# Optimization experiments

Measured on AMD Instinct MI355X. Metric: run time of the kernel, lower is better.

## Reference

```python
import jax, jax.numpy as jnp
import numpy as np

D_MODEL = 1024
N_HEAD = 16
DK = D_MODEL // N_HEAD


def setup_inputs() -> dict:
    key = jax.random.key(0)
    ks = jax.random.split(key, 9)
    s = 1.0 / np.sqrt(D_MODEL)
    x = jax.random.normal(ks[0], (2, 2048, D_MODEL), dtype=jnp.float32)
    def lin(kw, kb):
        W = jax.random.uniform(kw, (D_MODEL, D_MODEL), minval=-s, maxval=s, dtype=jnp.float32)
        b = jax.random.uniform(kb, (D_MODEL,), minval=-s, maxval=s, dtype=jnp.float32)
        return W, b
    Wq, bq = lin(ks[1], ks[2])
    Wk, bk = lin(ks[3], ks[4])
    Wv, bv = lin(ks[5], ks[6])
    Wo, bo = lin(ks[7], ks[8])
    return {"x": x, "Wq": Wq, "bq": bq, "Wk": Wk, "bk": bk,
            "Wv": Wv, "bv": bv, "Wo": Wo, "bo": bo}


def reference(x, Wq, bq, Wk, bk, Wv, bv, Wo, bo):
    B, T, _ = x.shape
    # nn.Linear: x @ W.T + b; reshape to (B, H, T, dk)
    def proj(W, b):
        y = x @ W.T + b
        return y.reshape(B, T, N_HEAD, DK).transpose(0, 2, 1, 3)
    Q = proj(Wq, bq)
    K = proj(Wk, bk)
    V = proj(Wv, bv)
    scores = jnp.einsum('bhqd,bhkd->bhqk', Q, K) / jnp.sqrt(jnp.float32(DK))
    attn = jax.nn.softmax(scores, axis=-1)
    out = jnp.einsum('bhqk,bhkd->bhqd', attn, V)
    out = out.transpose(0, 2, 1, 3).reshape(B, T, D_MODEL)
    return out @ Wo.T + bo
```

## Files before the change

kernel.cpp:

```cpp
#include <hip/hip_runtime.h>
#include <hip/hip_bf16.h>
#include <cstdint>

typedef unsigned short u16;
typedef __attribute__((ext_vector_type(8))) __bf16 bf16x8;
typedef __attribute__((ext_vector_type(8))) short s16x8;
typedef __attribute__((ext_vector_type(4))) short s16x4;
typedef __attribute__((ext_vector_type(4))) float f32x4;
typedef __attribute__((ext_vector_type(4))) unsigned u32x4;

#define T_SEQ 2048
#define D_MODEL 1024
#define MROWS 4096
#define QSCALE (0.125f * 1.44269504088896f)

__device__ __forceinline__ u16 f2bf(float f) {
  unsigned u = __builtin_bit_cast(unsigned, f);
  u += 0x7fffu + ((u >> 16) & 1u);
  return (u16)(u >> 16);
}

__device__ __forceinline__ unsigned cvt_pk_bf16(float lo, float hi) {
  unsigned r;
  asm("v_cvt_pk_bf16_f32 %0, %1, %2" : "=v"(r) : "v"(lo), "v"(hi));
  return r;
}

__device__ __forceinline__ void plswap(unsigned& a, unsigned& b) {
  asm("v_permlane32_swap_b32 %0, %1" : "+v"(a), "+v"(b));
  asm("v_permlane16_swap_b32 %0, %1" : "+v"(a), "+v"(b));
}

__device__ __forceinline__ void gld_lds16(const void* g, void* l) {
  __builtin_amdgcn_global_load_lds(
      (__attribute__((address_space(1))) void*)(uintptr_t)(g),
      (__attribute__((address_space(3))) void*)(uintptr_t)(l), 16, 0, 0);
}

__device__ __forceinline__ f32x4 mfma16(s16x8 a, s16x8 b, f32x4 c) {
  return __builtin_amdgcn_mfma_f32_16x16x32_bf16(
      __builtin_bit_cast(bf16x8, a), __builtin_bit_cast(bf16x8, b), c, 0, 0, 0);
}

__global__ __launch_bounds__(256) void cvt5(
    const float* __restrict__ x,
    const float* __restrict__ w0, const float* __restrict__ w1,
    const float* __restrict__ w2, const float* __restrict__ w3,
    u16* __restrict__ dx, u16* __restrict__ dw0, u16* __restrict__ dw1,
    u16* __restrict__ dw2, u16* __restrict__ dw3) {
  const int NX = (MROWS * D_MODEL) / 4;
  const int NW = (D_MODEL * D_MODEL) / 4;
  int i = blockIdx.x * 256 + threadIdx.x;
  const float* s;
  u16* d;
  int off;
  if (i < NX) {
    s = x; d = dx; off = i;
  } else {
    int j = i - NX;
    int r = j >> 18;
    off = j & (NW - 1);
    if (r == 0) { s = w0; d = dw0; }
    else if (r == 1) { s = w1; d = dw1; }
    else if (r == 2) { s = w2; d = dw2; }
    else { s = w3; d = dw3; }
  }
  float4 v = ((const float4*)s)[off];
  uint2 o;
  o.x = cvt_pk_bf16(v.x, v.y);
  o.y = cvt_pk_bf16(v.z, v.w);
  ((uint2*)d)[off] = o;
}

__global__ __launch_bounds__(512, 2) void gemm_qkv(const u16* __restrict__ A,
    const u16* __restrict__ Wf,
    const float* __restrict__ bq, const float* __restrict__ bk, const float* __restrict__ bv,
    u16* __restrict__ Qo, u16* __restrict__ Ko, u16* __restrict__ Vo) {
  __shared__ char smem[131072];

  const int t = threadIdx.x;
  const int lane = t & 63;
  const int lq = lane & 15, g = lane >> 4;
  const int w = t >> 6;
  const int wm = w >> 2, wn = w & 3;

  const int f = blockIdx.x;
  const int xcd = f & 7, i = f >> 3;
  const int by = (xcd & 3) * 4 + (i & 3);
  const int bx = (xcd >> 2) * 6 + (i >> 2);
  const int bm2 = by * 256, bn2 = bx * 256;

  auto stage = [&](int dst, int mat, int kh, int kt2) {
    const u16* gbase = mat ? Wf : A;
    const int gr0 = mat ? bn2 : bm2;
    char* lbase = smem + (((dst << 1) + mat) * 2 + kh) * 16384;
#pragma unroll
    for (int s = 0; s < 2; ++s) {
      const int idx = s * 512 + t;
      const int row = idx >> 2, c16 = idx & 3;
      const int gcol = kt2 * 64 + kh * 32 + 8 * (c16 ^ ((row >> 1) & 3));
      gld_lds16(gbase + (size_t)(gr0 + row) * D_MODEL + gcol, lbase + idx * 16);
    }
  };

  f32x4 acc[8][4] = {};
  const int swz4 = ((lq >> 1) & 3) << 4;
  const int aoff0 = (wm * 128 + lq) * 64 + ((g * 16) ^ swz4);
  const int boff0 = (wn * 64 + lq) * 64 + ((g * 16) ^ swz4);

  s16x8 bfr[4];
  auto loadB = [&](const char* cb) {
#pragma unroll
    for (int fc = 0; fc < 4; ++fc)
      bfr[fc] = *(const s16x8*)(cb + boff0 + fc * 1024);
  };
  auto quad = [&](const char* ca, int fr0) {
    s16x8 a[4];
#pragma unroll
    for (int ii = 0; ii < 4; ++ii)
      a[ii] = *(const s16x8*)(ca + aoff0 + (fr0 + ii) * 1024);
    __builtin_amdgcn_s_setprio(1);
#pragma unroll
    for (int ii = 0; ii < 4; ++ii)
#pragma unroll
      for (int fc = 0; fc < 4; ++fc)
        acc[fr0 + ii][fc] = mfma16(a[ii], bfr[fc], acc[fr0 + ii][fc]);
    __builtin_amdgcn_s_setprio(0);
  };

  stage(0, 0, 0, 0);
  stage(0, 1, 0, 0);
  stage(0, 0, 1, 0);
  stage(0, 1, 1, 0);

  const int NT = D_MODEL / 64;
#pragma unroll 1
  for (int kt = 0; kt < NT; ++kt) {
    const int d = kt & 1;
    const char* A0 = smem + (((d << 1) + 0) * 2 + 0) * 16384;
    const char* A1 = smem + (((d << 1) + 0) * 2 + 1) * 16384;
    const char* B0 = smem + (((d << 1) + 1) * 2 + 0) * 16384;
    const char* B1 = smem + (((d << 1) + 1) * 2 + 1) * 16384;
    const bool more = kt + 1 < NT;

    asm volatile("s_waitcnt vmcnt(4)" ::: "memory");
    __builtin_amdgcn_s_barrier();
    if (more) stage(d ^ 1, 0, 0, kt + 1);
    loadB(B0);
    quad(A0, 0);
    if (more) stage(d ^ 1, 1, 0, kt + 1);
    quad(A0, 4);

    if (more) asm volatile("s_waitcnt vmcnt(4)" ::: "memory");
    else      asm volatile("s_waitcnt vmcnt(0)" ::: "memory");
    __builtin_amdgcn_s_barrier();
    if (more) stage(d ^ 1, 0, 1, kt + 1);
    loadB(B1);
    quad(A1, 0);
    if (more) stage(d ^ 1, 1, 1, kt + 1);
    quad(A1, 4);
  }

  const int z = bn2 >> 10;
  const float* bias = z == 0 ? bq : (z == 1 ? bk : bv);
  u16* out = z == 0 ? Qo : (z == 1 ? Ko : Vo);
  const float scale = z == 0 ? QSCALE : 1.0f;
  const int bnl = bn2 & 1023;
#pragma unroll
  for (int fc = 0; fc < 4; ++fc) {
    const int col = bnl + wn * 64 + fc * 16 + lq;
    const float bvv = bias[col];
#pragma unroll
    for (int fr = 0; fr < 8; ++fr) {
      const int row0 = bm2 + wm * 128 + fr * 16 + g * 4;
#pragma unroll
      for (int r = 0; r < 4; ++r)
        out[(size_t)(row0 + r) * D_MODEL + col] = f2bf((acc[fr][fc][r] + bvv) * scale);
    }
  }
}

template <int BN, class Epi>
__device__ __forceinline__ void gemm_pipe(const u16* __restrict__ A,
    const u16* __restrict__ Bw, const int K, const int bm, const int bn, Epi epi) {
  constexpr int NJ = BN / 32;
  constexpr int VM = 2 + BN / 64;
  constexpr int AB = 8192;
  __shared__ char lds[3][AB + BN * 64];
  const int t = threadIdx.x;
  const int lane = t & 63;
  const int lq = lane & 15, g = lane >> 4;
  const int w = t >> 6;
  const int wr = w >> 1, wc = w & 1;

  f32x4 acc[4][NJ] = {};
  const int NT = K >> 5;

  auto stage = [&](int buf, int kt) {
    const int k0 = kt << 5;
#pragma unroll
    for (int s = 0; s < 2; ++s) {
      const int idx = s * 256 + t;
      const int kk = idx >> 7, mm = idx & 127;
      gld_lds16(A + (size_t)(bm + mm) * K + (k0 + kk * 8), &lds[buf][(idx & ~63) * 16]);
    }
#pragma unroll
    for (int s = 0; s < BN / 64; ++s) {
      const int idx = s * 256 + t;
      const int kk = idx / BN, nn = idx % BN;
      gld_lds16(Bw + (size_t)(bn + nn) * K + (k0 + kk * 8), &lds[buf][AB + (idx & ~63) * 16]);
    }
  };

  auto compute = [&](int buf) {
    const char* la = &lds[buf][0];
    const char* lb = &lds[buf][AB];
    s16x8 af[4], bfr[NJ];
#pragma unroll
    for (int i = 0; i < 4; ++i)
      af[i] = *(const s16x8*)(la + g * 2048 + (wr * 64 + i * 16 + lq) * 16);
#pragma unroll
    for (int j = 0; j < NJ; ++j)
      bfr[j] = *(const s16x8*)(lb + g * (BN * 16) + (wc * (BN / 2) + j * 16 + lq) * 16);
    __builtin_amdgcn_s_setprio(1);
#pragma unroll
    for (int i = 0; i < 4; ++i)
#pragma unroll
      for (int j = 0; j < NJ; ++j)
        acc[i][j] = mfma16(af[i], bfr[j], acc[i][j]);
    __builtin_amdgcn_s_setprio(0);
  };

  auto vmwait = [&]() {
    if constexpr (VM == 4) asm volatile("s_waitcnt vmcnt(4)" ::: "memory");
    else asm volatile("s_waitcnt vmcnt(3)" ::: "memory");
  };

  stage(0, 0);
  stage(1, 1);
  int b0 = 0, b1 = 1, b2 = 2;
#pragma unroll 1
  for (int kt = 0; kt < NT - 2; ++kt) {
    vmwait();
    __builtin_amdgcn_s_barrier();
    stage(b2, kt + 2);
    compute(b0);
    const int tmp = b0; b0 = b1; b1 = b2; b2 = tmp;
  }
  vmwait();
  __builtin_amdgcn_s_barrier();
  compute(b0);
  asm volatile("s_waitcnt vmcnt(0)" ::: "memory");
  __builtin_amdgcn_s_barrier();
  compute(b1);

  epi(acc, lq, g, wr, wc);
}

__global__ __launch_bounds__(256) void gemm_out(const u16* __restrict__ A,
    const u16* __restrict__ W, const float* __restrict__ bias, float* __restrict__ C) {
  const int f = blockIdx.x;
  const int xcd = f & 7, i = f >> 3;
  const int by = xcd * 4 + (i & 3);
  const int bx = i >> 2;
  const int bm = by * 128, bn = bx * 64;

  gemm_pipe<64>(A, W, D_MODEL, bm, bn,
      [&](f32x4 (&acc)[4][2], int lq, int g, int wr, int wc) {
#pragma unroll
        for (int j = 0; j < 2; ++j) {
          const int col = bn + wc * 32 + j * 16 + lq;
          const float bvv = bias[col];
#pragma unroll
          for (int i2 = 0; i2 < 4; ++i2) {
            const int row0 = bm + wr * 64 + i2 * 16 + g * 4;
#pragma unroll
            for (int r = 0; r < 4; ++r)
              C[(size_t)(row0 + r) * D_MODEL + col] = acc[i2][j][r] + bvv;
          }
        }
      });
}

__global__ __launch_bounds__(512, 4) void attn_kernel(const u16* __restrict__ Qw,
    const u16* __restrict__ Kw, const u16* __restrict__ Vw, u16* __restrict__ AO) {
  __shared__ char smem[34816];
  char* Ks = smem;
  char* Vs = smem + 16384;

  const int t = threadIdx.x;
  const int w = t >> 6, lane = t & 63;
  const int lq = lane & 15, g = lane >> 4;
  const int qh = w >> 1, kh = w & 1;

  const int flat = blockIdx.y * 16 + blockIdx.x;
  const int xcd = flat & 7, idx = flat >> 3;
  const int bh = xcd * 4 + (idx & 3);
  const int qt = idx >> 2;
  const int b = bh >> 4, h = bh & 15;
  const size_t headoff = (size_t)b * T_SEQ * D_MODEL + h * 64;
  const int swz = (lq & 7) << 4;

  s16x8 qf[2][2];
#pragma unroll
  for (int qb = 0; qb < 2; ++qb) {
    const u16* qptr = Qw + headoff + (size_t)(qt * 128 + qh * 32 + qb * 16 + lq) * D_MODEL;
#pragma unroll
    for (int hb = 0; hb < 2; ++hb)
      qf[qb][hb] = *(const s16x8*)(qptr + hb * 32 + g * 8);
  }

  const int kkey = t >> 3, kslot = t & 7;
  auto stageK = [&](int buf, int kt) {
    const int d0 = 8 * (kslot ^ (kkey & 7));
    gld_lds16(Kw + headoff + (size_t)(kt * 64 + kkey) * D_MODEL + d0,
              Ks + buf * 8192 + (t & ~63) * 16);
  };

  const int kp = t & 31, dg = t >> 5;
  auto loadV = [&](int kt, s16x4& va, s16x4& vb2) {
    const u16* gv = Vw + headoff + (size_t)(kt * 64 + 2 * kp) * D_MODEL + 4 * dg;
    va = *(const s16x4*)gv;
    vb2 = *(const s16x4*)(gv + D_MODEL);
  };
  auto writeV = [&](int buf, s16x4 va, s16x4 vb2) {
    char* vbase = Vs + buf * 8192;
#pragma unroll
    for (int j = 0; j < 4; ++j) {
      const int d = 4 * dg + j;
      const unsigned u = (unsigned)(u16)va[j] | ((unsigned)(u16)vb2[j] << 16);
      *(unsigned*)(vbase + d * 128 + ((4 * kp) ^ ((d & 7) << 4))) = u;
    }
  };

  f32x4 o[4][2] = {};
  f32x4 lsum[2] = {};

  s16x4 va, vb2;
  stageK(0, 0);
  loadV(0, va, vb2);

  int cur = 0;
#pragma unroll 1
  for (int kt = 0; kt < T_SEQ / 64; ++kt) {
    asm volatile("s_waitcnt vmcnt(0)" ::: "memory");
    writeV(cur, va, vb2);
    __syncthreads();
    const bool more = kt + 1 < T_SEQ / 64;
    if (more) { stageK(cur ^ 1, kt + 1); loadV(kt + 1, va, vb2); }

    const char* kb_ = Ks + cur * 8192 + kh * 4096;
    f32x4 s[2][2] = {};
    __builtin_amdgcn_s_setprio(1);
#pragma unroll
    for (int kb = 0; kb < 2; ++kb)
#pragma unroll
      for (int hb = 0; hb < 2; ++hb) {
        const s16x8 kf = *(const s16x8*)(kb_ + (16 * kb + lq) * 128 + ((64 * hb + 16 * g) ^ swz));
#pragma unroll
        for (int qb = 0; qb < 2; ++qb)
          s[kb][qb] = mfma16(kf, qf[qb][hb], s[kb][qb]);
      }
    __builtin_amdgcn_s_setprio(0);

#pragma unroll
    for (int kb = 0; kb < 2; ++kb)
#pragma unroll
      for (int qb = 0; qb < 2; ++qb) {
#pragma unroll
        for (int r = 0; r < 4; ++r) s[kb][qb][r] = __builtin_amdgcn_exp2f(s[kb][qb][r]);
        lsum[qb] += s[kb][qb];
      }

    s16x8 pb[2];
#pragma unroll
    for (int qb = 0; qb < 2; ++qb) {
      unsigned a0 = cvt_pk_bf16(s[0][qb][0], s[0][qb][1]);
      unsigned a1 = cvt_pk_bf16(s[0][qb][2], s[0][qb][3]);
      unsigned b0 = cvt_pk_bf16(s[1][qb][0], s[1][qb][1]);
      unsigned b1 = cvt_pk_bf16(s[1][qb][2], s[1][qb][3]);
      plswap(a0, b0);
      plswap(a1, b1);
      u32x4 pk = {a0, a1, b0, b1};
      pb[qb] = __builtin_bit_cast(s16x8, pk);
    }

    const char* vb_ = Vs + cur * 8192;
    __builtin_amdgcn_s_setprio(1);
#pragma unroll
    for (int f = 0; f < 4; ++f) {
      const s16x8 av = *(const s16x8*)(vb_ + (16 * f + lq) * 128 + ((64 * kh + 16 * g) ^ swz));
#pragma unroll
      for (int qb = 0; qb < 2; ++qb)
        o[f][qb] = mfma16(av, pb[qb], o[f][qb]);
    }
    __builtin_amdgcn_s_setprio(0);
    cur ^= 1;
  }

  float rsq[2];
#pragma unroll
  for (int qb = 0; qb < 2; ++qb) {
    float r_ = lsum[qb][0] + lsum[qb][1] + lsum[qb][2] + lsum[qb][3];
    r_ += __shfl_xor(r_, 16);
    r_ += __shfl_xor(r_, 32);
    rsq[qb] = r_;
  }

  __syncthreads();
  char* obuf = smem;
  float* rbuf = (float*)(smem + 32768);
  if (kh == 1) {
#pragma unroll
    for (int f = 0; f < 4; ++f)
#pragma unroll
      for (int qb = 0; qb < 2; ++qb)
        *(f32x4*)(obuf + qh * 8192 + lane * 128 + (((f * 2 + qb) * 16) ^ ((lane & 7) << 4))) =
            o[f][qb];
    rbuf[qh * 128 + lane * 2 + 0] = rsq[0];
    rbuf[qh * 128 + lane * 2 + 1] = rsq[1];
  }
  __syncthreads();
  if (kh == 0) {
#pragma unroll
    for (int f = 0; f < 4; ++f)
#pragma unroll
      for (int qb = 0; qb < 2; ++qb)
        o[f][qb] += *(const f32x4*)(obuf + qh * 8192 + lane * 128 +
                                    (((f * 2 + qb) * 16) ^ ((lane & 7) << 4)));
    const float inv0 = 1.0f / (rsq[0] + rbuf[qh * 128 + lane * 2 + 0]);
    const float inv1 = 1.0f / (rsq[1] + rbuf[qh * 128 + lane * 2 + 1]);
#pragma unroll
    for (int qb = 0; qb < 2; ++qb) {
      const float inv = qb ? inv1 : inv0;
      u16* orow = AO + headoff + (size_t)(qt * 128 + qh * 32 + qb * 16 + lq) * D_MODEL;
#pragma unroll
      for (int f = 0; f < 4; ++f) {
        uint2 ov;
        ov.x = cvt_pk_bf16(o[f][qb][0] * inv, o[f][qb][1] * inv);
        ov.y = cvt_pk_bf16(o[f][qb][2] * inv, o[f][qb][3] * inv);
        *(uint2*)(orow + 16 * f + 4 * g) = ov;
      }
    }
  }
}

extern "C" void kernel_launch(void* const* d_in, const int* in_sizes, int n_in,
                              void* d_out, int out_size, void* d_ws, size_t ws_size,
                              hipStream_t stream) {
  const float* x  = (const float*)d_in[0];
  const float* Wq = (const float*)d_in[1];
  const float* bq = (const float*)d_in[2];
  const float* Wk = (const float*)d_in[3];
  const float* bk = (const float*)d_in[4];
  const float* Wv = (const float*)d_in[5];
  const float* bv = (const float*)d_in[6];
  const float* Wo = (const float*)d_in[7];
  const float* bo = (const float*)d_in[8];

  char* ws = (char*)d_ws;
  const size_t MB = 1u << 20;
  u16* x_bf  = (u16*)(ws + 0 * MB);
  u16* AO    = x_bf;
  u16* Wq_bf = (u16*)(ws + 8 * MB);
  u16* Wk_bf = (u16*)(ws + 10 * MB);
  u16* Wv_bf = (u16*)(ws + 12 * MB);
  u16* Wo_bf = (u16*)(ws + 14 * MB);
  u16* Qs  = (u16*)(ws + 16 * MB);
  u16* Ksb = (u16*)(ws + 24 * MB);
  u16* Vsb = (u16*)(ws + 32 * MB);

  const int NCVT = (MROWS * D_MODEL + 4 * D_MODEL * D_MODEL) / 4;
  cvt5<<<NCVT / 256, 256, 0, stream>>>(x, Wq, Wk, Wv, Wo,
                                       x_bf, Wq_bf, Wk_bf, Wv_bf, Wo_bf);

  gemm_qkv<<<192, 512, 0, stream>>>(x_bf, Wq_bf, bq, bk, bv, Qs, Ksb, Vsb);
  attn_kernel<<<dim3(16, 32), 512, 0, stream>>>(Qs, Ksb, Vsb, AO);
  gemm_out<<<512, 256, 0, stream>>>(AO, Wo_bf, bo, (float*)d_out);
}
```

Baseline: 117.7 us.

## Restructure QKV GEMM into triple-buffered 32-wide K pipeline with less LDS

Replaces the double-buffered 64-wide K-tile loop in the QKV projection GEMM with a three-stage ring of 32-wide K tiles, cutting shared memory from 128KB to 96KB. Each iteration loads A and B fragments, issues prefetch of the tile two steps ahead, and splits the MFMA work into two halves separated by barriers. The aim is deeper prefetch and lower LDS use. In exchange it adds more barriers per unit of K work and relies on the vmcnt accounting being right.

```diff
diff --git a/kernel.cpp b/kernel.cpp
--- a/kernel.cpp
+++ b/kernel.cpp
@@ -76,7 +76,7 @@
     const u16* __restrict__ Wf,
     const float* __restrict__ bq, const float* __restrict__ bk, const float* __restrict__ bv,
     u16* __restrict__ Qo, u16* __restrict__ Ko, u16* __restrict__ Vo) {
-  __shared__ char smem[131072];
+  __shared__ char smem[98304];
 
   const int t = threadIdx.x;
   const int lane = t & 63;
@@ -90,15 +90,15 @@
   const int bx = (xcd >> 2) * 6 + (i >> 2);
   const int bm2 = by * 256, bn2 = bx * 256;
 
-  auto stage = [&](int dst, int mat, int kh, int kt2) {
+  auto stage = [&](int b, int mat, int kt) {
     const u16* gbase = mat ? Wf : A;
     const int gr0 = mat ? bn2 : bm2;
-    char* lbase = smem + (((dst << 1) + mat) * 2 + kh) * 16384;
+    char* lbase = smem + b * 32768 + mat * 16384;
 #pragma unroll
     for (int s = 0; s < 2; ++s) {
       const int idx = s * 512 + t;
       const int row = idx >> 2, c16 = idx & 3;
-      const int gcol = kt2 * 64 + kh * 32 + 8 * (c16 ^ ((row >> 1) & 3));
+      const int gcol = kt * 32 + 8 * (c16 ^ ((row >> 1) & 3));
       gld_lds16(gbase + (size_t)(gr0 + row) * D_MODEL + gcol, lbase + idx * 16);
     }
   };
@@ -108,57 +108,49 @@
   const int aoff0 = (wm * 128 + lq) * 64 + ((g * 16) ^ swz4);
   const int boff0 = (wn * 64 + lq) * 64 + ((g * 16) ^ swz4);
 
-  s16x8 bfr[4];
-  auto loadB = [&](const char* cb) {
-#pragma unroll
-    for (int fc = 0; fc < 4; ++fc)
-      bfr[fc] = *(const s16x8*)(cb + boff0 + fc * 1024);
-  };
-  auto quad = [&](const char* ca, int fr0) {
-    s16x8 a[4];
-#pragma unroll
-    for (int ii = 0; ii < 4; ++ii)
-      a[ii] = *(const s16x8*)(ca + aoff0 + (fr0 + ii) * 1024);
-    __builtin_amdgcn_s_setprio(1);
-#pragma unroll
-    for (int ii = 0; ii < 4; ++ii)
-#pragma unroll
-      for (int fc = 0; fc < 4; ++fc)
-        acc[fr0 + ii][fc] = mfma16(a[ii], bfr[fc], acc[fr0 + ii][fc]);
-    __builtin_amdgcn_s_setprio(0);
-  };
-
-  stage(0, 0, 0, 0);
-  stage(0, 1, 0, 0);
-  stage(0, 0, 1, 0);
-  stage(0, 1, 1, 0);
-
-  const int NT = D_MODEL / 64;
+  stage(0, 0, 0); stage(0, 1, 0);
+  stage(1, 0, 1); stage(1, 1, 1);
+  asm volatile("s_waitcnt vmcnt(4)" ::: "memory");
+  __builtin_amdgcn_s_barrier();
+
+  const int NT = 32;
 #pragma unroll 1
   for (int kt = 0; kt < NT; ++kt) {
-    const int d = kt & 1;
-    const char* A0 = smem + (((d << 1) + 0) * 2 + 0) * 16384;
-    const char* A1 = smem + (((d << 1) + 0) * 2 + 1) * 16384;
-    const char* B0 = smem + (((d << 1) + 1) * 2 + 0) * 16384;
-    const char* B1 = smem + (((d << 1) + 1) * 2 + 1) * 16384;
-    const bool more = kt + 1 < NT;
-
-    asm volatile("s_waitcnt vmcnt(4)" ::: "memory");
+    const int cb = kt % 3, nb = (kt + 2) % 3;
+    const char* ca = smem + cb * 32768;
+    const char* cbB = smem + cb * 32768 + 16384;
+    const bool st = kt + 2 < NT;
+
+    s16x8 af[4], bfr[4];
+#pragma unroll
+    for (int x = 0; x < 4; ++x) af[x] = *(const s16x8*)(ca + aoff0 + x * 1024);
+#pragma unroll
+    for (int x = 0; x < 4; ++x) bfr[x] = *(const s16x8*)(cbB + boff0 + x * 1024);
+    if (st) stage(nb, 0, kt + 2);
     __builtin_amdgcn_s_barrier();
-    if (more) stage(d ^ 1, 0, 0, kt + 1);
-    loadB(B0);
-    quad(A0, 0);
-    if (more) stage(d ^ 1, 1, 0, kt + 1);
-    quad(A0, 4);
-
-    if (more) asm volatile("s_waitcnt vmcnt(4)" ::: "memory");
-    else      asm volatile("s_waitcnt vmcnt(0)" ::: "memory");
+    __builtin_amdgcn_s_setprio(1);
+#pragma unroll
+    for (int fr = 0; fr < 4; ++fr)
+#pragma unroll
+      for (int fc = 0; fc < 4; ++fc)
+        acc[fr][fc] = mfma16(af[fr], bfr[fc], acc[fr][fc]);
+    __builtin_amdgcn_s_setprio(0);
     __builtin_amdgcn_s_barrier();
-    if (more) stage(d ^ 1, 0, 1, kt + 1);
-    loadB(B1);
-    quad(A1, 0);
-    if (more) stage(d ^ 1, 1, 1, kt + 1);
-    quad(A1, 4);
+
+#pragma unroll
+    for (int x = 0; x < 4; ++x) af[x] = *(const s16x8*)(ca + aoff0 + (4 + x) * 1024);
+    if (st) stage(nb, 1, kt + 2);
+    __builtin_amdgcn_s_barrier();
+    __builtin_amdgcn_s_setprio(1);
+#pragma unroll
+    for (int fr = 0; fr < 4; ++fr)
+#pragma unroll
+      for (int fc = 0; fc < 4; ++fc)
+        acc[4 + fr][fc] = mfma16(af[fr], bfr[fc], acc[4 + fr][fc]);
+    __builtin_amdgcn_s_setprio(0);
+    if (kt < NT - 2) asm volatile("s_waitcnt vmcnt(4)" ::: "memory");
+    else if (kt == NT - 2) asm volatile("s_waitcnt vmcnt(0)" ::: "memory");
+    __builtin_amdgcn_s_barrier();
   }
 
   const int z = bn2 >> 10;
```

Measured after the change: 121.1 us. 2.9% more time.
